# Kernel optimization log

Measured on AMD Instinct MI355X. Metric: run time of the kernel, lower is better.

Reference implementation:

```python
import jax, jax.numpy as jnp
import numpy as np

SCALE = 100.0
ALPHA_MEM = 0.9
ALPHA_MEM_OUT = 0.9
ALPHA_R = 0.85
ALPHA_X = 0.95
ALPHA_P = 0.95
ALPHA_D = 0.95
WMIN = 0.0
WMAX = 2.0


@jax.custom_vjp
def spike_fn(x):
    # SurrGradSpike.forward: heaviside(x)
    return (x > 0).astype(x.dtype)

def _spike_fwd(x):
    return spike_fn(x), x

def _spike_bwd(x, g):
    # SurrGradSpike.backward: g / (scale*|x| + 1)^2
    return (g / (SCALE * jnp.abs(x) + 1.0) ** 2,)

spike_fn.defvjp(_spike_fwd, _spike_bwd)


def setup_inputs() -> dict:
    key = jax.random.key(0)
    ks = jax.random.split(key, 8)
    B, T, NI, N, NO, D = 8, 64, 256, 512, 32, 4
    inputs = jax.random.normal(ks[0], (B, T, NI), jnp.float32)
    w = jax.random.normal(ks[1], (N, N), jnp.float32) * (0.1 / np.sqrt(N))
    w_in = jax.random.normal(ks[2], (NI, N), jnp.float32) * (1.0 / np.sqrt(NI))
    w_out = jax.random.normal(ks[3], (N, NO), jnp.float32) * (1.0 / np.sqrt(N))
    # each synapse (e,o) assigned exactly one delay bin -> one-hot delay map (D,N,N)
    delay_idx = jax.random.randint(ks[4], (N, N), 0, D)
    dmap = jax.nn.one_hot(delay_idx, D, axis=0, dtype=jnp.float32)
    delays = jnp.array([1, 2, 3, 5], jnp.int32)
    w_signs = jnp.where(jnp.arange(N) < (4 * N) // 5, 1.0, -1.0).astype(jnp.float32)
    p = jax.random.uniform(ks[5], (N,), jnp.float32, minval=-0.5, maxval=0.5)
    A_p = jax.random.uniform(ks[6], (N, N), jnp.float32, minval=0.0, maxval=1e-3)
    A_d = jax.random.uniform(ks[7], (N, N), jnp.float32, minval=0.0, maxval=1e-3)
    return dict(inputs=inputs, w=w, w_in=w_in, w_out=w_out, dmap=dmap,
                delays=delays, w_signs=w_signs, p=p, A_p=A_p, A_d=A_d)


def _snn_forward(inputs, w, w_in, w_out, dmap, delays, w_signs, p, A_p, A_d):
    B, T, _ = inputs.shape
    N = w.shape[0]
    dt = inputs.dtype
    # epoch state
    inp = jnp.einsum('btc,cn->btn', inputs, w_in)          # (B,T,N)
    W = dmap * (w_signs[:, None] * jnp.abs(w))             # (D,N,N)
    p_depr = (p < 0).astype(dt)

    mem = jnp.zeros((B, N), dt)
    w_p = jnp.zeros((B, N), dt)
    x_bar = jnp.zeros((B, N), dt)
    u_pot = jnp.zeros((B, N), dt)
    u_dep = jnp.zeros((B, N), dt)
    w_stdp = jnp.ones((B, N, N), dt)
    rec_out = jnp.zeros((T, B, N), dt)
    rec_wp = jnp.zeros((T, B, N), dt)
    rec_xb = jnp.zeros((T, B, N), dt)

    def step(carry, xt):
        mem, w_p, x_bar, u_pot, u_dep, w_stdp, rec_out, rec_wp, rec_xb = carry
        t, inp_t = xt
        # mark_spikes + record_state (records pre-update values)
        spike = spike_fn(mem - 1.0)
        rec_out = rec_out.at[t].set(spike)
        rec_wp = rec_wp.at[t].set(w_p)
        rec_xb = rec_xb.at[t].set(x_bar)
        # delayed gathers; negative torch indices hit zero-initialized tail -> %T
        idx = (t - delays) % T
        out_del = jnp.take(rec_out, idx, axis=0)           # (D,B,N)
        wp_del = jnp.take(rec_wp, idx, axis=0)
        xb_del = jnp.take(rec_xb, idx, axis=0)
        # synaptic input
        syn_p = out_del * (1.0 + wp_del)
        syn = jnp.einsum('dbe,deo,beo->bo', syn_p, W, w_stdp)
        # STP
        dw_p = spike * p * (1.0 + p_depr * w_p)
        w_p = w_p * ALPHA_R + dw_p
        # STDP (uses pre-update u_dep/u_pot/mem)
        X = jnp.einsum('dbe,deo->beo', out_del, dmap)
        dW_dep = X * A_d[None] * jax.nn.relu(u_dep)[:, None, :]
        xbar_d = jnp.einsum('dbe,deo->beo', xb_del, dmap)
        dW_pot = xbar_d * A_p[None] * (jax.lax.stop_gradient(spike) * jax.nn.relu(u_pot))[:, None, :]
        x_bar = ALPHA_X * x_bar + (1.0 - ALPHA_X) * jax.lax.stop_gradient(spike)
        u_pot = ALPHA_P * u_pot + (1.0 - ALPHA_P) * mem
        u_dep = ALPHA_D * u_dep + (1.0 - ALPHA_D) * mem
        w_stdp = jnp.clip(w_stdp + dW_pot - dW_dep, WMIN, WMAX)
        # membrane integration with spike reset (detached)
        mem = ALPHA_MEM * mem + inp_t + syn - jax.lax.stop_gradient(spike)
        return (mem, w_p, x_bar, u_pot, u_dep, w_stdp, rec_out, rec_wp, rec_xb), None

    carry = (mem, w_p, x_bar, u_pot, u_dep, w_stdp, rec_out, rec_wp, rec_xb)
    xs = (jnp.arange(T), jnp.swapaxes(inp, 0, 1))
    carry, _ = jax.lax.scan(jax.checkpoint(step), carry, xs)
    rec_out = carry[6]                                     # (T,B,N)
    # readout: leaky integrator over projected spikes
    h2 = jnp.einsum('btn,no->bto', jnp.swapaxes(rec_out, 0, 1), w_out)

    def ro_step(o, h):
        o = ALPHA_MEM_OUT * o + h
        return o, o

    _, readout = jax.lax.scan(ro_step, jnp.zeros((B, h2.shape[-1]), dt),
                              jnp.swapaxes(h2, 0, 1))
    return jnp.swapaxes(readout, 0, 1)                     # (B,T,n_outputs)


def reference(inputs, w, w_in, w_out, dmap, delays, w_signs, p, A_p, A_d):
    return _snn_forward(inputs, w, w_in, w_out, dmap, delays, w_signs, p, A_p, A_d)
```

## Files before the change

kernel.cpp:

```cpp
#include <hip/hip_runtime.h>
#include <stdint.h>


#define B  8
#define T  64
#define NI 256
#define NN 512
#define NO 32
#define DD 4

#define NBLK 256
#define TPB  256
#define OPB  16
#define SPL  32
#define EPAD 516

#define REC_ELEMS (T*B*NN)
#define MAGIC  0x534E4E31u

#define C_CNT   0
#define C_GCNT  8
#define C_PAR   9
#define C_HDR   10
#define C_DONE  16

__device__ __forceinline__ unsigned long long rec_load(const unsigned long long* p) {
    return __hip_atomic_load(p, __ATOMIC_RELAXED, __HIP_MEMORY_SCOPE_AGENT);
}
__device__ __forceinline__ void rec_store(unsigned long long* p, unsigned long long v) {
    __hip_atomic_store(p, v, __ATOMIC_RELAXED, __HIP_MEMORY_SCOPE_AGENT);
}
__device__ __forceinline__ unsigned ctrl_ld(const unsigned* p) {
    return __hip_atomic_load(p, __ATOMIC_RELAXED, __HIP_MEMORY_SCOPE_AGENT);
}
__device__ __forceinline__ void ctrl_st(unsigned* p, unsigned v) {
    __hip_atomic_store(p, v, __ATOMIC_RELAXED, __HIP_MEMORY_SCOPE_AGENT);
}
__device__ __forceinline__ bool unwritten(unsigned long long v, unsigned runpar) {
    return ((unsigned)v >> 31) != runpar;
}
__device__ __forceinline__ unsigned long long poll_written(
        const unsigned long long* src, unsigned long long v, unsigned runpar) {
    int guard = 0;
    while (unwritten(v, runpar)) {
        if (guard >= 2) __builtin_amdgcn_s_sleep(1);
        v = rec_load(src);
        if (++guard > (1 << 18)) break;
    }
    return v;
}

#define BAR_LDS() do {                                      \
    asm volatile("s_waitcnt lgkmcnt(0)" ::: "memory");      \
    __builtin_amdgcn_s_barrier();                           \
    asm volatile("" ::: "memory");                          \
} while (0)

__global__ __launch_bounds__(TPB, 1)
void snn_main(const float* __restrict__ inputs,
              const float* __restrict__ w,
              const float* __restrict__ w_in,
              const float* __restrict__ w_out,
              const float* __restrict__ dmap,
              const int*   __restrict__ delays,
              const float* __restrict__ w_signs,
              const float* __restrict__ p,
              const float* __restrict__ A_p,
              const float* __restrict__ A_d,
              unsigned long long* __restrict__ rec,
              float* __restrict__ h2buf,
              unsigned* __restrict__ ctrl,
              float* __restrict__ out)
{
    __shared__ float2 sxq[DD*EPAD];
    __shared__ float  inp_s[T*OPB];
    __shared__ float  red[64];
    __shared__ unsigned int spikebits_s[T];
    __shared__ float  wout16_s[OPB*NO];
    __shared__ float  h2_s[T*NO];
    __shared__ int    last_s;

    const int tid     = threadIdx.x;
    const int bid     = blockIdx.x;
    const int b       = bid & 7;
    const int chunk   = bid >> 3;
    const int o_base  = chunk * OPB;
    const int o_local = tid & 15;
    const int e_grp   = tid >> 4;
    const int o       = o_base + o_local;

    unsigned runpar;
    if (ctrl_ld(ctrl + C_HDR) != MAGIC) {
        {
            unsigned long long* base = rec + (size_t)bid * (REC_ELEMS / NBLK);
            #pragma unroll
            for (int i = 0; i < REC_ELEMS / NBLK / TPB; ++i)
                rec_store(base + i*TPB + tid, 0x0000000080000000ull);
        }
        {
            unsigned* hb = (unsigned*)h2buf + (size_t)bid * ((B*T*NO) / NBLK);
            #pragma unroll
            for (int i = 0; i < (B*T*NO) / NBLK / TPB + 1; ++i) {
                const int k = i*TPB + tid;
                if (k < (B*T*NO) / NBLK)
                    ctrl_st(hb + k, 0u);
            }
        }
        if (bid == 0 && tid < 10) ctrl_st(ctrl + tid, 0u);
        __syncthreads();
        if (tid == 0) ctrl_st(ctrl + C_DONE + bid, MAGIC);
        {
            int guard = 0;
            while (ctrl_ld(ctrl + C_DONE + tid) != MAGIC) {
                __builtin_amdgcn_s_sleep(2);
                if (++guard > (1 << 20)) break;
            }
        }
        __syncthreads();
        runpar = 0u;
    } else {
        runpar = ctrl_ld(ctrl + C_PAR);
    }

    if (tid < OPB) {
        rec_store(rec + (size_t)(0*B + b)*NN + o_base + tid,
                  (unsigned long long)(runpar << 31));
    }
    if (tid == 0) spikebits_s[0] = 0u;

    float wv[SPL], ap[SPL], ad[SPL], ws[SPL];
    int   laddr[SPL];
    #pragma unroll
    for (int i = 0; i < SPL; ++i) {
        const int e = e_grp + 16*i;
        wv[i] = w_signs[e] * fabsf(w[e*NN + o]);
        ap[i] = A_p[e*NN + o];
        ad[i] = A_d[e*NN + o];
        int d = 0;
        if (dmap[1*NN*NN + e*NN + o] != 0.0f) d = 1;
        if (dmap[2*NN*NN + e*NN + o] != 0.0f) d = 2;
        if (dmap[3*NN*NN + e*NN + o] != 0.0f) d = 3;
        ws[i]    = 1.0f;
        laddr[i] = (d*EPAD + e) * 8;
    }
    int del[DD];
    #pragma unroll
    for (int d = 0; d < DD; ++d) del[d] = delays[d];

    {
        float* win = (float*)sxq;
        for (int k = tid; k < NI*OPB; k += TPB) {
            const int c = k >> 4, oo = k & 15;
            win[c*OPB + oo] = w_in[c*NN + o_base + oo];
        }
        __syncthreads();
        #pragma unroll
        for (int j = 0; j < 4; ++j) {
            const int tj = e_grp*4 + j;
            const float* inrow = inputs + (size_t)(b*T + tj)*NI;
            float a = 0.f;
            for (int c = 0; c < NI; ++c) a += inrow[c] * win[c*OPB + o_local];
            inp_s[tj*OPB + o_local] = a;
        }
        __syncthreads();
    }

    #pragma unroll
    for (int d = 0; d < DD; ++d) {
        sxq[d*EPAD + tid]       = make_float2(0.f, 0.f);
        sxq[d*EPAD + 256 + tid] = make_float2(0.f, 0.f);
    }
    __syncthreads();

    float mem = 0.f, w_p = 0.f, x_bar = 0.f, u_pot = 0.f, u_dep = 0.f;
    const float p_o  = p[o];
    const float pd_o = (p_o < 0.f) ? 1.f : 0.f;

    unsigned long long pf[DD][2];
    const int stage_ord[DD] = {1, 2, 3, 0};

    for (int t = 0; t < T; ++t) {
        if (t + 1 < T) {
            #pragma unroll
            for (int d = 0; d < DD; ++d) {
                if (t + 1 >= del[d]) {
                    const int s = (t + 1 - del[d]) & 63;
                    const unsigned long long* src = rec + (size_t)(s*B + b)*NN + tid;
                    pf[d][0] = rec_load(src);
                    pf[d][1] = rec_load(src + 256);
                }
            }
        }

        const float spike = (mem > 1.0f) ? 1.0f : 0.0f;
        const float pg  = spike * fmaxf(u_pot, 0.f);
        const float udr = fmaxf(u_dep, 0.f);
        float2 v[SPL];
        float acc = 0.f;
        #pragma unroll
        for (int i = 0; i < SPL; ++i) {
            v[i] = *(const float2*)((const char*)sxq + laddr[i]);
            acc = fmaf(v[i].x, wv[i]*ws[i], acc);
        }
        float a2 = acc + __shfl_xor(acc, 16);
        a2 += __shfl_xor(a2, 32);
        if ((tid & 63) < 16) red[(tid >> 6)*16 + o_local] = a2;
        BAR_LDS();
        const float syn = red[o_local] + red[16 + o_local] + red[32 + o_local] + red[48 + o_local];

        const float wp_new = 0.85f*w_p + spike * p_o * (1.f + pd_o*w_p);
        const float xb_new = 0.95f*x_bar + 0.05f*spike;
        u_pot = 0.95f*u_pot + 0.05f*mem;
        u_dep = 0.95f*u_dep + 0.05f*mem;
        mem   = 0.9f*mem + inp_s[t*OPB + o_local] + syn - spike;
        w_p   = wp_new;
        x_bar = xb_new;

        if (t + 1 < T && tid < OPB) {
            const float spike1 = (mem > 1.0f) ? 1.0f : 0.0f;
            const float sp = spike1 * (1.f + w_p);
            const unsigned int xu = __float_as_uint(x_bar) | (spike1 != 0.f ? 0x80000000u : 0u);
            const unsigned int lo = __float_as_uint(sp) | (runpar << 31);
            const unsigned long long pk = ((unsigned long long)xu << 32) | lo;
            rec_store(rec + (size_t)((t+1)*B + b)*NN + o_base + tid, pk);
            const unsigned long long bal = __ballot(spike1 != 0.0f);
            if (tid == 0) spikebits_s[t+1] = (unsigned int)bal;
        }

        #pragma unroll
        for (int i = 0; i < SPL; ++i) {
            const unsigned int xu = __float_as_uint(v[i].y);
            const float dep = ((int)xu < 0) ? ad[i]*udr : 0.f;
            const float pot = (ap[i]*pg) * fabsf(v[i].y);
            ws[i] = fminf(fmaxf(ws[i] + pot - dep, 0.f), 2.f);
        }

        if (t + 1 < T) {
            #pragma unroll
            for (int j = 0; j < DD; ++j) {
                const int d = stage_ord[j];
                unsigned long long v0 = (unsigned long long)(runpar << 31);
                unsigned long long v1 = v0;
                if (t + 1 >= del[d]) {
                    const int s = (t + 1 - del[d]) & 63;
                    const unsigned long long* src = rec + (size_t)(s*B + b)*NN + tid;
                    v0 = poll_written(src,       pf[d][0], runpar);
                    v1 = poll_written(src + 256, pf[d][1], runpar);
                }
                sxq[d*EPAD + tid] =
                    make_float2(__uint_as_float((unsigned)v0 & 0x7fffffffu),
                                __uint_as_float((unsigned)(v0 >> 32)));
                sxq[d*EPAD + 256 + tid] =
                    make_float2(__uint_as_float((unsigned)v1 & 0x7fffffffu),
                                __uint_as_float((unsigned)(v1 >> 32)));
            }
        }
        BAR_LDS();
    }

    for (int k = tid; k < OPB*NO; k += TPB)
        wout16_s[k] = w_out[(o_base + (k >> 5))*NO + (k & 31)];
    __syncthreads();

    const int g  = tid >> 5;
    const int oo = tid & 31;
    #pragma unroll
    for (int j = 0; j < 8; ++j) {
        const int t = g*8 + j;
        const unsigned int bits = spikebits_s[t];
        float a = 0.f;
        #pragma unroll
        for (int i = 0; i < OPB; ++i)
            if (bits & (1u << i)) a += wout16_s[i*NO + oo];
        if (a != 0.f) atomicAdd(h2buf + ((size_t)b*T + t)*NO + oo, a);
    }
    __threadfence();
    __syncthreads();
    if (tid == 0) last_s = (atomicAdd(ctrl + C_CNT + b, 1u) == 31u) ? 1 : 0;
    __syncthreads();

    if (last_s) {
        __threadfence();
        #pragma unroll
        for (int j = 0; j < 8; ++j) {
            const int t = g*8 + j;
            h2_s[t*NO + oo] = __hip_atomic_load(h2buf + ((size_t)b*T + t)*NO + oo,
                                                __ATOMIC_RELAXED, __HIP_MEMORY_SCOPE_AGENT);
        }
        __syncthreads();
        if (tid < NO) {
            float st = 0.f;
            for (int t = 0; t < T; ++t) {
                st = 0.9f*st + h2_s[t*NO + tid];
                out[((size_t)b*T + t)*NO + tid] = st;
            }
        }
    }

    if (tid == 0) {
        const unsigned gar = __hip_atomic_fetch_add(ctrl + C_GCNT, 1u,
                                                    __ATOMIC_ACQ_REL, __HIP_MEMORY_SCOPE_AGENT);
        if (gar == NBLK - 1) {
            for (int i = 0; i < 8; ++i) ctrl_st(ctrl + C_CNT + i, 0u);
            ctrl_st(ctrl + C_GCNT, 0u);
            ctrl_st(ctrl + C_PAR, runpar ^ 1u);
            ctrl_st(ctrl + C_HDR, MAGIC);
        }
    }
}

extern "C" void kernel_launch(void* const* d_in, const int* in_sizes, int n_in,
                              void* d_out, int out_size, void* d_ws, size_t ws_size,
                              hipStream_t stream)
{
    const float* inputs  = (const float*)d_in[0];
    const float* w       = (const float*)d_in[1];
    const float* w_in    = (const float*)d_in[2];
    const float* w_out   = (const float*)d_in[3];
    const float* dmap    = (const float*)d_in[4];
    const int*   delays  = (const int*)  d_in[5];
    const float* w_signs = (const float*)d_in[6];
    const float* p       = (const float*)d_in[7];
    const float* A_p     = (const float*)d_in[8];
    const float* A_d     = (const float*)d_in[9];

    char* wsb = (char*)d_ws;
    unsigned long long* rec = (unsigned long long*)wsb;
    float* h2buf = (float*)(wsb + (size_t)REC_ELEMS*8);
    unsigned* ctrl = (unsigned*)(wsb + (size_t)REC_ELEMS*8 + (size_t)B*T*NO*4);

    hipLaunchKernelGGL(snn_main, dim3(NBLK), dim3(TPB), 0, stream,
                       inputs, w, w_in, w_out, dmap, delays, w_signs, p, A_p, A_d,
                       rec, h2buf, ctrl, (float*)d_out);
}
```

Before: 277.3 us.

## Double threads per block to halve per-thread synapse work and staging loads

Raises the block size from 256 to 512 threads, so each thread holds 16 presynaptic synapses instead of 32 and stages one rec element per delay instead of two. The cross-wave reduction widens from 4 to 8 partial sums. Prefetch loads for delays other than 1 become plain non-atomic loads. The aim is to shorten the serial per-timestep critical path, at the cost of more threads in each block barrier and a larger reduction.

```diff
diff --git a/kernel.cpp b/kernel.cpp
--- a/kernel.cpp
+++ b/kernel.cpp
@@ -10,9 +10,10 @@
 #define DD 4
 
 #define NBLK 256
-#define TPB  256
+#define TPB  512
 #define OPB  16
-#define SPL  32
+#define EGR  32
+#define SPL  16
 #define EPAD 516
 
 #define REC_ELEMS (T*B*NN)
@@ -26,6 +27,9 @@
 
 __device__ __forceinline__ unsigned long long rec_load(const unsigned long long* p) {
     return __hip_atomic_load(p, __ATOMIC_RELAXED, __HIP_MEMORY_SCOPE_AGENT);
+}
+__device__ __forceinline__ unsigned long long rec_load_plain(const unsigned long long* p) {
+    return *p;
 }
 __device__ __forceinline__ void rec_store(unsigned long long* p, unsigned long long v) {
     __hip_atomic_store(p, v, __ATOMIC_RELAXED, __HIP_MEMORY_SCOPE_AGENT);
@@ -56,7 +60,7 @@
     asm volatile("" ::: "memory");                          \
 } while (0)
 
-__global__ __launch_bounds__(TPB, 1)
+__global__ __launch_bounds__(TPB, 2)
 void snn_main(const float* __restrict__ inputs,
               const float* __restrict__ w,
               const float* __restrict__ w_in,
@@ -74,7 +78,7 @@
 {
     __shared__ float2 sxq[DD*EPAD];
     __shared__ float  inp_s[T*OPB];
-    __shared__ float  red[64];
+    __shared__ float  red[8*OPB];
     __shared__ unsigned int spikebits_s[T];
     __shared__ float  wout16_s[OPB*NO];
     __shared__ float  h2_s[T*NO];
@@ -99,17 +103,12 @@
         }
         {
             unsigned* hb = (unsigned*)h2buf + (size_t)bid * ((B*T*NO) / NBLK);
-            #pragma unroll
-            for (int i = 0; i < (B*T*NO) / NBLK / TPB + 1; ++i) {
-                const int k = i*TPB + tid;
-                if (k < (B*T*NO) / NBLK)
-                    ctrl_st(hb + k, 0u);
-            }
+            if (tid < (B*T*NO) / NBLK) ctrl_st(hb + tid, 0u);
         }
         if (bid == 0 && tid < 10) ctrl_st(ctrl + tid, 0u);
         __syncthreads();
         if (tid == 0) ctrl_st(ctrl + C_DONE + bid, MAGIC);
-        {
+        if (tid < NBLK) {
             int guard = 0;
             while (ctrl_ld(ctrl + C_DONE + tid) != MAGIC) {
                 __builtin_amdgcn_s_sleep(2);
@@ -132,7 +131,7 @@
     int   laddr[SPL];
     #pragma unroll
     for (int i = 0; i < SPL; ++i) {
-        const int e = e_grp + 16*i;
+        const int e = e_grp + EGR*i;
         wv[i] = w_signs[e] * fabsf(w[e*NN + o]);
         ap[i] = A_p[e*NN + o];
         ad[i] = A_d[e*NN + o];
@@ -149,14 +148,16 @@
 
     {
         float* win = (float*)sxq;
-        for (int k = tid; k < NI*OPB; k += TPB) {
+        #pragma unroll
+        for (int q = 0; q < NI*OPB/TPB; ++q) {
+            const int k = q*TPB + tid;
             const int c = k >> 4, oo = k & 15;
             win[c*OPB + oo] = w_in[c*NN + o_base + oo];
         }
         __syncthreads();
         #pragma unroll
-        for (int j = 0; j < 4; ++j) {
-            const int tj = e_grp*4 + j;
+        for (int j = 0; j < T/EGR; ++j) {
+            const int tj = e_grp*(T/EGR) + j;
             const float* inrow = inputs + (size_t)(b*T + tj)*NI;
             float a = 0.f;
             for (int c = 0; c < NI; ++c) a += inrow[c] * win[c*OPB + o_local];
@@ -166,17 +167,15 @@
     }
 
     #pragma unroll
-    for (int d = 0; d < DD; ++d) {
-        sxq[d*EPAD + tid]       = make_float2(0.f, 0.f);
-        sxq[d*EPAD + 256 + tid] = make_float2(0.f, 0.f);
-    }
+    for (int d = 0; d < DD; ++d)
+        sxq[d*EPAD + tid] = make_float2(0.f, 0.f);
     __syncthreads();
 
     float mem = 0.f, w_p = 0.f, x_bar = 0.f, u_pot = 0.f, u_dep = 0.f;
     const float p_o  = p[o];
     const float pd_o = (p_o < 0.f) ? 1.f : 0.f;
 
-    unsigned long long pf[DD][2];
+    unsigned long long pf[DD];
     const int stage_ord[DD] = {1, 2, 3, 0};
 
     for (int t = 0; t < T; ++t) {
@@ -186,8 +185,7 @@
                 if (t + 1 >= del[d]) {
                     const int s = (t + 1 - del[d]) & 63;
                     const unsigned long long* src = rec + (size_t)(s*B + b)*NN + tid;
-                    pf[d][0] = rec_load(src);
-                    pf[d][1] = rec_load(src + 256);
+                    pf[d] = (del[d] == 1) ? rec_load(src) : rec_load_plain(src);
                 }
             }
         }
@@ -206,7 +204,9 @@
         a2 += __shfl_xor(a2, 32);
         if ((tid & 63) < 16) red[(tid >> 6)*16 + o_local] = a2;
         BAR_LDS();
-        const float syn = red[o_local] + red[16 + o_local] + red[32 + o_local] + red[48 + o_local];
+        float syn = 0.f;
+        #pragma unroll
+        for (int k = 0; k < 8; ++k) syn += red[k*16 + o_local];
 
         const float wp_new = 0.85f*w_p + spike * p_o * (1.f + pd_o*w_p);
         const float xb_new = 0.95f*x_bar + 0.05f*spike;
@@ -240,33 +240,27 @@
             for (int j = 0; j < DD; ++j) {
                 const int d = stage_ord[j];
                 unsigned long long v0 = (unsigned long long)(runpar << 31);
-                unsigned long long v1 = v0;
                 if (t + 1 >= del[d]) {
                     const int s = (t + 1 - del[d]) & 63;
                     const unsigned long long* src = rec + (size_t)(s*B + b)*NN + tid;
-                    v0 = poll_written(src,       pf[d][0], runpar);
-                    v1 = poll_written(src + 256, pf[d][1], runpar);
+                    v0 = poll_written(src, pf[d], runpar);
                 }
                 sxq[d*EPAD + tid] =
                     make_float2(__uint_as_float((unsigned)v0 & 0x7fffffffu),
                                 __uint_as_float((unsigned)(v0 >> 32)));
-                sxq[d*EPAD + 256 + tid] =
-                    make_float2(__uint_as_float((unsigned)v1 & 0x7fffffffu),
-                                __uint_as_float((unsigned)(v1 >> 32)));
             }
         }
         BAR_LDS();
     }
 
-    for (int k = tid; k < OPB*NO; k += TPB)
-        wout16_s[k] = w_out[(o_base + (k >> 5))*NO + (k & 31)];
+    if (tid < OPB*NO) wout16_s[tid] = w_out[(o_base + (tid >> 5))*NO + (tid & 31)];
     __syncthreads();
 
     const int g  = tid >> 5;
     const int oo = tid & 31;
     #pragma unroll
-    for (int j = 0; j < 8; ++j) {
-        const int t = g*8 + j;
+    for (int j = 0; j < 4; ++j) {
+        const int t = g*4 + j;
         const unsigned int bits = spikebits_s[t];
         float a = 0.f;
         #pragma unroll
@@ -282,8 +276,8 @@
     if (last_s) {
         __threadfence();
         #pragma unroll
-        for (int j = 0; j < 8; ++j) {
-            const int t = g*8 + j;
+        for (int j = 0; j < 4; ++j) {
+            const int t = g*4 + j;
             h2_s[t*NO + oo] = __hip_atomic_load(h2buf + ((size_t)b*T + t)*NO + oo,
                                                 __ATOMIC_RELAXED, __HIP_MEMORY_SCOPE_AGENT);
         }
```

Result: faster. 223.3 us (median of 3 runs) (-19.5%).
